# Kernel optimization log

Hardware: AMD Instinct MI355X
Metric: run time of the kernel (lower is better)

Reference implementation:

```python
import jax, jax.numpy as jnp
import numpy as np

N, E, H, ED, TD = 10000, 320000, 128, 64, 32

def _lin(x, w, b):
    return x @ w + b

def _ln(x, g, b, eps=1e-5):
    m = jnp.mean(x, axis=-1, keepdims=True)
    v = jnp.var(x, axis=-1, keepdims=True)
    return (x - m) * jax.lax.rsqrt(v + eps) * g + b

def _mlp(x, w1, b1, g, bt, w2, b2):
    y = jax.nn.silu(_ln(_lin(x, w1, b1), g, bt))
    return _lin(y, w2, b2)

def setup_inputs() -> dict:
    key = jax.random.key(0)
    ks = jax.random.split(key, 32)
    s = 0.02
    nrm = lambda k, shp: jax.random.normal(k, shp, jnp.float32) * s
    d = {}
    d['h'] = jax.random.normal(ks[0], (N, H), jnp.float32)
    d['edge_attr'] = jax.random.normal(ks[1], (E, ED), jnp.float32)
    d['edge_time_emb'] = jax.random.normal(ks[2], (E, TD), jnp.float32)
    d['edge_index'] = jax.random.randint(ks[3], (2, E), 0, N)
    # edge_emb + edge_norm
    d['w_ee'] = nrm(ks[4], (ED + TD, ED)); d['b_ee'] = jnp.zeros((ED,), jnp.float32)
    d['g_en'] = jnp.ones((ED + TD,), jnp.float32); d['bt_en'] = jnp.zeros((ED + TD,), jnp.float32)
    # node_linear / bond_linear
    d['w_nl'] = nrm(ks[5], (H, H)); d['b_nl'] = jnp.zeros((H,), jnp.float32)
    d['w_bl'] = nrm(ks[6], (ED, H)); d['b_bl'] = jnp.zeros((H,), jnp.float32)
    # bond_linear_left/right, node_linear_left/right
    d['w_bll'] = nrm(ks[7], (ED, H)); d['b_bll'] = jnp.zeros((H,), jnp.float32)
    d['w_blr'] = nrm(ks[8], (ED, H)); d['b_blr'] = jnp.zeros((H,), jnp.float32)
    d['w_nll'] = nrm(ks[9], (H, H)); d['b_nll'] = jnp.zeros((H,), jnp.float32)
    d['w_nlr'] = nrm(ks[10], (H, H)); d['b_nlr'] = jnp.zeros((H,), jnp.float32)
    # left / right MLPs: Linear(2H,H), LayerNorm(H), SiLU, Linear(H,H)
    d['mlpl_w1'] = nrm(ks[11], (2 * H, H)); d['mlpl_b1'] = jnp.zeros((H,), jnp.float32)
    d['mlpl_g'] = jnp.ones((H,), jnp.float32); d['mlpl_bt'] = jnp.zeros((H,), jnp.float32)
    d['mlpl_w2'] = nrm(ks[12], (H, H)); d['mlpl_b2'] = jnp.zeros((H,), jnp.float32)
    d['mlpr_w1'] = nrm(ks[13], (2 * H, H)); d['mlpr_b1'] = jnp.zeros((H,), jnp.float32)
    d['mlpr_g'] = jnp.ones((H,), jnp.float32); d['mlpr_bt'] = jnp.zeros((H,), jnp.float32)
    d['mlpr_w2'] = nrm(ks[14], (H, H)); d['mlpr_b2'] = jnp.zeros((H,), jnp.float32)
    # layer_norm(3H) + bond_out: Linear(3H,H), SiLU, Linear(H,ED)
    d['g_ln'] = jnp.ones((3 * H,), jnp.float32); d['bt_ln'] = jnp.zeros((3 * H,), jnp.float32)
    d['w_o1'] = nrm(ks[15], (3 * H, H)); d['b_o1'] = jnp.zeros((H,), jnp.float32)
    d['w_o2'] = nrm(ks[16], (H, ED)); d['b_o2'] = jnp.zeros((ED,), jnp.float32)
    return d

def reference(h, edge_attr, edge_time_emb, edge_index,
              w_ee, b_ee, g_en, bt_en, w_nl, b_nl, w_bl, b_bl,
              w_bll, b_bll, w_blr, b_blr, w_nll, b_nll, w_nlr, b_nlr,
              mlpl_w1, mlpl_b1, mlpl_g, mlpl_bt, mlpl_w2, mlpl_b2,
              mlpr_w1, mlpr_b1, mlpr_g, mlpr_bt, mlpr_w2, mlpr_b2,
              g_ln, bt_ln, w_o1, b_o1, w_o2, b_o2):
    src, dst = edge_index[0], edge_index[1]
    n = h.shape[0]
    # edge_attr = edge_emb(edge_norm(cat([edge_attr, edge_time_emb])))
    ea = _lin(_ln(jnp.concatenate([edge_attr, edge_time_emb], axis=-1), g_en, bt_en), w_ee, b_ee)
    # node linears applied per-node then gathered (same math as gather-then-linear)
    x_i = _lin(h, w_nll, b_nll)[src]            # [E, H]
    x_j = _lin(h, w_nlr, b_nlr)[dst]            # [E, H]
    edge_i = _lin(ea, w_bll, b_bll)             # [E, H]
    edge_j = _lin(ea, w_blr, b_blr)             # [E, H]
    inter_i = _mlp(jnp.concatenate([edge_i, x_i], axis=-1), mlpl_w1, mlpl_b1, mlpl_g, mlpl_bt, mlpl_w2, mlpl_b2)
    inter_j = _mlp(jnp.concatenate([edge_j, x_j], axis=-1), mlpr_w1, mlpr_b1, mlpr_g, mlpr_bt, mlpr_w2, mlpr_b2)
    # scatter_sum to nodes, then regather on the same index
    inter_i = jax.ops.segment_sum(inter_i, src, num_segments=n)[src]
    inter_j = jax.ops.segment_sum(inter_j, dst, num_segments=n)[dst]
    h_node = _lin(h, w_nl, b_nl)
    h_bond = jnp.concatenate([inter_i + inter_j, h_node[src] + h_node[dst], _lin(ea, w_bl, b_bl)], axis=-1)  # [E, 3H]
    h_bond = _ln(h_bond, g_ln, bt_ln)
    out = _lin(jax.nn.silu(_lin(h_bond, w_o1, b_o1)), w_o2, b_o2)  # [E, ED]
    return out
```

## Files before the change

### kernel.cpp

```cpp
#include <hip/hip_runtime.h>
#include <math.h>


using u16 = unsigned short;
using u32 = unsigned int;
typedef __attribute__((ext_vector_type(8))) short  short8;
typedef __attribute__((ext_vector_type(4))) float  f32x4;
typedef __attribute__((ext_vector_type(4))) u32    uint4v;
typedef __attribute__((ext_vector_type(2))) u32    uint2v;

constexpr int NN = 10000;
constexpr int EE = 320000;
constexpr int MAXDEG = 96;

__device__ __forceinline__ float b2f(u16 v) {
  return __builtin_bit_cast(float, (u32)v << 16);
}
__device__ __forceinline__ u16 f2b(float f) {
  u32 u = __builtin_bit_cast(u32, f);
  return (u16)((u + 0x7fffu + ((u >> 16) & 1u)) >> 16);
}
__device__ __forceinline__ uint2v pack4(f32x4 v) {
  uint2v r;
  r.x = (u32)f2b(v[0]) | ((u32)f2b(v[1]) << 16);
  r.y = (u32)f2b(v[2]) | ((u32)f2b(v[3]) << 16);
  return r;
}

struct Params {
  const void* h; const void* edge_attr; const void* te;
  const int* eidx;
  const int* flag;
  const u16 *b_ee, *g_en, *bt_en;
  const u16 *b_nl, *b_bl, *b_bll, *b_blr, *b_nll, *b_nlr;
  const u16 *l_b1, *l_g, *l_bt, *l_b2;
  const u16 *r_b1, *r_g, *r_bt, *r_b2;
  const u16 *g_ln, *bt_ln, *b_o1, *b_o2;
  const u16 *w_eeT, *w_blT, *w_bllT, *w_blrT, *w_nlT, *w_nllT, *w_nlrT;
  const u16 *l_w1T, *l_w2T, *r_w1T, *r_w2T, *o1T, *o2T;
  u16 *a_nll, *a_nlr, *h_node, *ea_ws;
  u32 *cnt0, *cnt1, *elist0, *elist1;
  u16 *accb_i, *accb_j;
  float *accf_i, *accf_j;
  u16 *inter0, *inter1;
  int amode;
  void *out;
};

__global__ __launch_bounds__(256) void k_sniff(const u16* p, int* flag)
{
  __shared__ int c;
  if (threadIdx.x == 0) c = 0;
  __syncthreads();
  u16 v = p[threadIdx.x * 2];
  int e = (v >> 7) & 0xff;
  if (e >= 100 && e <= 140) atomicAdd(&c, 1);
  __syncthreads();
  if (threadIdx.x == 0) *flag = (c >= 200) ? 1 : 0;
}

template<int K, int CT, int RT>
__device__ __forceinline__ void wave_gemm(const u16* A, int SA,
                                          const u16* __restrict__ BT,
                                          f32x4 (&acc)[RT][CT], int n0)
{
  const int lane = threadIdx.x & 63;
  const int quad = lane >> 4, l16 = lane & 15;
#pragma unroll
  for (int kt = 0; kt < K / 32; ++kt) {
    const int k0 = kt * 32 + quad * 8;
    short8 b[CT];
#pragma unroll
    for (int c = 0; c < CT; ++c)
      b[c] = *(const short8*)(BT + (size_t)(n0 + c * 16 + l16) * K + k0);
#pragma unroll
    for (int rt = 0; rt < RT; ++rt) {
      short8 av = *(const short8*)(A + (rt * 16 + l16) * SA + k0);
#pragma unroll
      for (int c = 0; c < CT; ++c)
        acc[rt][c] = __builtin_amdgcn_mfma_f32_16x16x32_bf16(av, b[c], acc[rt][c], 0, 0, 0);
    }
  }
}

template<int CT, int RT, bool SILU>
__device__ __forceinline__ void epi_lds(f32x4 (&acc)[RT][CT], u16* O, int SO,
                                        int outc0, const u16* __restrict__ bias,
                                        int biasc0)
{
  const int lane = threadIdx.x & 63;
  const int quad = lane >> 4, l16 = lane & 15;
#pragma unroll
  for (int c = 0; c < CT; ++c) {
    float bv = b2f(bias[biasc0 + c * 16 + l16]);
#pragma unroll
    for (int rt = 0; rt < RT; ++rt) {
#pragma unroll
      for (int r = 0; r < 4; ++r) {
        float v = acc[rt][c][r] + bv;
        if (SILU) v = v / (1.f + __expf(-v));
        O[(rt * 16 + quad * 4 + r) * SO + outc0 + c * 16 + l16] = f2b(v);
      }
    }
  }
}

template<int D, int ROWS, bool SILU>
__device__ __forceinline__ void ln_rows(u16* buf, int S,
                                        const u16* __restrict__ g,
                                        const u16* __restrict__ bt, float* red)
{
  constexpr int P = 256 / ROWS;
  constexpr int C = D / P;
  const int t = threadIdx.x;
  const int row = t / P, p = t % P;
  u16* r = buf + row * S + p * C;
  float s = 0.f, ss = 0.f;
#pragma unroll 8
  for (int i = 0; i < C; ++i) { float v = b2f(r[i]); s += v; ss += v * v; }
  red[row * 2 * P + p] = s;
  red[row * 2 * P + P + p] = ss;
  __syncthreads();
  float S1 = 0.f, S2 = 0.f;
#pragma unroll
  for (int q = 0; q < P; ++q) {
    S1 += red[row * 2 * P + q];
    S2 += red[row * 2 * P + P + q];
  }
  const float mean = S1 / (float)D;
  const float var  = S2 / (float)D - mean * mean;
  const float rstd = rsqrtf(var + 1e-5f);
#pragma unroll 8
  for (int i = 0; i < C; ++i) {
    int col = p * C + i;
    float v = (b2f(r[i]) - mean) * rstd * b2f(g[col]) + b2f(bt[col]);
    if (SILU) v = v / (1.f + __expf(-v));
    r[i] = f2b(v);
  }
  __syncthreads();
}

struct TDesc { const void* s; u16* d; int K; int N; };
struct TArgs { TDesc t[34]; const int* flag; };

__global__ __launch_bounds__(256) void k_transpose(TArgs a)
{
  const int flag = *a.flag;
  TDesc dsc = a.t[blockIdx.y];
  const int total = dsc.K * dsc.N;
  for (int i = blockIdx.x * 256 + threadIdx.x; i < total; i += gridDim.x * 256) {
    int n = i / dsc.K;
    int k = i - n * dsc.K;
    size_t si = (size_t)k * dsc.N + n;
    dsc.d[i] = flag ? ((const u16*)dsc.s)[si] : f2b(((const float*)dsc.s)[si]);
  }
}

__global__ __launch_bounds__(256) void k_hist(const int* eidx, u32* cnt0,
                                              u32* elist0, u32* cnt1, u32* elist1)
{
  int e = blockIdx.x * 256 + threadIdx.x;
  if (e >= EE) return;
  int n0 = eidx[e];
  u32 p0 = atomicAdd(&cnt0[n0], 1u);
  if (p0 < MAXDEG) elist0[(size_t)n0 * MAXDEG + p0] = (u32)e;
  int n1 = eidx[EE + e];
  u32 p1 = atomicAdd(&cnt1[n1], 1u);
  if (p1 < MAXDEG) elist1[(size_t)n1 * MAXDEG + p1] = (u32)e;
}

__global__ __launch_bounds__(256) void k_node(Params a)
{
  __shared__ __align__(16) u16 hs[64 * 136];
  const int tid = threadIdx.x, w = tid >> 6;
  const int n0 = blockIdx.x * 64;
  const int flag = *a.flag;
  if (flag) {
    for (int c = tid; c < 1024; c += 256) {
      int row = c >> 4, cc = c & 15;
      int node = n0 + row;
      uint4v v = {};
      if (node < NN) v = *(const uint4v*)((const u16*)a.h + (size_t)node * 128 + cc * 8);
      *(uint4v*)&hs[row * 136 + cc * 8] = v;
    }
  } else {
    for (int c = tid; c < 2048; c += 256) {
      int row = c >> 5, cc = c & 31;
      int node = n0 + row;
      uint2v pk = {};
      if (node < NN) {
        f32x4 fv = *(const f32x4*)((const float*)a.h + (size_t)node * 128 + cc * 4);
        pk = pack4(fv);
      }
      *(uint2v*)&hs[row * 136 + cc * 4] = pk;
    }
  }
  __syncthreads();
  const u16* wT[3] = { a.w_nllT, a.w_nlrT, a.w_nlT };
  const u16* bs[3] = { a.b_nll, a.b_nlr, a.b_nl };
  u16* os[3] = { a.a_nll, a.a_nlr, a.h_node };
  const int lane = tid & 63, quad = lane >> 4, l16 = lane & 15;
#pragma unroll 1
  for (int m = 0; m < 3; ++m) {
    f32x4 acc[4][2] = {};
    wave_gemm<128, 2, 4>(hs, 136, wT[m], acc, w * 32);
#pragma unroll
    for (int c = 0; c < 2; ++c) {
      int col = w * 32 + c * 16 + l16;
      float bv = b2f(bs[m][col]);
#pragma unroll
      for (int rt = 0; rt < 4; ++rt) {
#pragma unroll
        for (int r = 0; r < 4; ++r) {
          int node = n0 + rt * 16 + quad * 4 + r;
          if (node < NN) os[m][(size_t)node * 128 + col] = f2b(acc[rt][c][r] + bv);
        }
      }
    }
  }
}

__global__ __launch_bounds__(256) void k_ea(Params a)
{
  __shared__ __align__(16) u16 u[64 * 104];
  __shared__ __align__(16) u16 eas[64 * 72];
  __shared__ float red[512];
  const int tid = threadIdx.x, w = tid >> 6;
  const int e0 = blockIdx.x * 64;
  const int flag = *a.flag;
  if (flag) {
    for (int c = tid; c < 512; c += 256) {
      int row = c >> 3, cc = c & 7;
      *(uint4v*)&u[row * 104 + cc * 8] =
          *(const uint4v*)((const u16*)a.edge_attr + (size_t)(e0 + row) * 64 + cc * 8);
    }
    {
      int row = tid >> 2, cc = tid & 3;
      *(uint4v*)&u[row * 104 + 64 + cc * 8] =
          *(const uint4v*)((const u16*)a.te + (size_t)(e0 + row) * 32 + cc * 8);
    }
  } else {
    for (int c = tid; c < 1024; c += 256) {
      int row = c >> 4, cc = c & 15;
      f32x4 fv = *(const f32x4*)((const float*)a.edge_attr + (size_t)(e0 + row) * 64 + cc * 4);
      *(uint2v*)&u[row * 104 + cc * 4] = pack4(fv);
    }
    for (int c = tid; c < 512; c += 256) {
      int row = c >> 3, cc = c & 7;
      f32x4 fv = *(const f32x4*)((const float*)a.te + (size_t)(e0 + row) * 32 + cc * 4);
      *(uint2v*)&u[row * 104 + 64 + cc * 4] = pack4(fv);
    }
  }
  __syncthreads();
  ln_rows<96, 64, false>(u, 104, a.g_en, a.bt_en, red);
  {
    f32x4 acc[4][1] = {};
    wave_gemm<96, 1, 4>(u, 104, a.w_eeT, acc, w * 16);
    epi_lds<1, 4, false>(acc, eas, 72, w * 16, a.b_ee, w * 16);
  }
  __syncthreads();
  for (int c = tid; c < 512; c += 256) {
    int row = c >> 3, cc = c & 7;
    *(uint4v*)(a.ea_ws + (size_t)(e0 + row) * 64 + cc * 8) =
        *(const uint4v*)&eas[row * 72 + cc * 8];
  }
}

template<bool ATOMIC>
__global__ __launch_bounds__(256) void k_mlp(
    const u16* __restrict__ ea_ws, const int* __restrict__ eidx_side,
    const u16* __restrict__ an, const u16* __restrict__ wbT,
    const u16* __restrict__ bb, const u16* __restrict__ w1T,
    const u16* __restrict__ b1, const u16* __restrict__ gg,
    const u16* __restrict__ bt, const u16* __restrict__ w2T,
    const u16* __restrict__ b2, u16* __restrict__ inter,
    float* __restrict__ accf)
{
  __shared__ __align__(16) u16 u[64 * 264];
  __shared__ __align__(16) u16 eas[64 * 72];
  __shared__ float red[512];
  __shared__ int sidx[64];
  const int tid = threadIdx.x, w = tid >> 6;
  const int e0 = blockIdx.x * 64;
  const int lane = tid & 63, quad = lane >> 4, l16 = lane & 15;

  if (tid < 64) sidx[tid] = eidx_side[e0 + tid];
  for (int c = tid; c < 512; c += 256) {
    int row = c >> 3, cc = c & 7;
    *(uint4v*)&eas[row * 72 + cc * 8] =
        *(const uint4v*)(ea_ws + (size_t)(e0 + row) * 64 + cc * 8);
  }
  __syncthreads();
  for (int c = tid; c < 1024; c += 256) {
    int row = c >> 4, cc = c & 15;
    *(uint4v*)&u[row * 264 + 128 + cc * 8] =
        *(const uint4v*)(an + (size_t)sidx[row] * 128 + cc * 8);
  }
  {
    f32x4 acc[4][2] = {};
    wave_gemm<64, 2, 4>(eas, 72, wbT, acc, w * 32);
    epi_lds<2, 4, false>(acc, u, 264, w * 32, bb, w * 32);
  }
  __syncthreads();
  {
    f32x4 acc[4][2] = {};
    wave_gemm<256, 2, 4>(u, 264, w1T, acc, w * 32);
    __syncthreads();
    epi_lds<2, 4, false>(acc, u, 264, w * 32, b1, w * 32);
  }
  __syncthreads();
  ln_rows<128, 64, true>(u, 264, gg, bt, red);
  {
    f32x4 acc[4][2] = {};
    wave_gemm<128, 2, 4>(u, 264, w2T, acc, w * 32);
    if (ATOMIC) {
#pragma unroll
      for (int c = 0; c < 2; ++c) {
        int col = w * 32 + c * 16 + l16;
        float bias = b2f(b2[col]);
#pragma unroll
        for (int rt = 0; rt < 4; ++rt)
#pragma unroll
          for (int r = 0; r < 4; ++r) {
            int row = rt * 16 + quad * 4 + r;
            unsafeAtomicAdd(accf + (size_t)sidx[row] * 128 + col,
                            acc[rt][c][r] + bias);
          }
      }
    } else {
      epi_lds<2, 4, false>(acc, u, 264, 128 + w * 32, b2, w * 32);
      __syncthreads();
      for (int c = tid; c < 1024; c += 256) {
        int row = c >> 4, cc = c & 15;
        *(uint4v*)(inter + (size_t)(e0 + row) * 128 + cc * 8) =
            *(const uint4v*)&u[row * 264 + 128 + cc * 8];
      }
    }
  }
}

__global__ __launch_bounds__(256) void k_nodesum(const u16* __restrict__ inter,
                                                 const u32* __restrict__ cnt,
                                                 const u32* __restrict__ elist,
                                                 u16* __restrict__ accb)
{
  const int wv = (blockIdx.x * 256 + threadIdx.x) >> 6;
  const int lane = threadIdx.x & 63;
  if (wv >= NN) return;
  u32 deg = cnt[wv];
  if (deg > MAXDEG) deg = MAXDEG;
  const u32* el = elist + (size_t)wv * MAXDEG;
  float s0 = 0.f, s1 = 0.f;
  for (u32 d = 0; d < deg; ++d) {
    u32 e = el[d];
    u32 v = *(const u32*)(inter + (size_t)e * 128 + lane * 2);
    s0 += b2f((u16)(v & 0xffff));
    s1 += b2f((u16)(v >> 16));
  }
  *(u32*)(accb + (size_t)wv * 128 + lane * 2) = (u32)f2b(s0) | ((u32)f2b(s1) << 16);
}

__global__ __launch_bounds__(256) void k_stage2(Params a)
{
  __shared__ __align__(16) u16 bond[32 * 392];
  __shared__ __align__(16) u16 eas[32 * 72];
  __shared__ float red[512];
  __shared__ int sidx[2][32];
  const int tid = threadIdx.x, w = tid >> 6;
  const int e0 = blockIdx.x * 32;
  const int flag = *a.flag;
  const int lane = tid & 63, quad = lane >> 4, l16 = lane & 15;

  if (tid < 64) {
    int side = tid >> 5, i = tid & 31;
    sidx[side][i] = a.eidx[(size_t)side * EE + e0 + i];
  }
  {
    int row = tid >> 3, cc = tid & 7;
    *(uint4v*)&eas[row * 72 + cc * 8] =
        *(const uint4v*)(a.ea_ws + (size_t)(e0 + row) * 64 + cc * 8);
  }
  __syncthreads();
  if (a.amode) {
    for (int c = tid; c < 1024; c += 256) {
      int row = c >> 5, cc = c & 31;
      uint2v vi = *(const uint2v*)(a.accb_i + (size_t)sidx[0][row] * 128 + cc * 4);
      uint2v vj = *(const uint2v*)(a.accb_j + (size_t)sidx[1][row] * 128 + cc * 4);
      uint2v ov;
#pragma unroll
      for (int q = 0; q < 2; ++q) {
        float lo = b2f((u16)(vi[q] & 0xffff)) + b2f((u16)(vj[q] & 0xffff));
        float hi = b2f((u16)(vi[q] >> 16))    + b2f((u16)(vj[q] >> 16));
        ov[q] = (u32)f2b(lo) | ((u32)f2b(hi) << 16);
      }
      *(uint2v*)&bond[row * 392 + cc * 4] = ov;
    }
  } else {
    for (int c = tid; c < 1024; c += 256) {
      int row = c >> 5, cc = c & 31;
      f32x4 vi = *(const f32x4*)(a.accf_i + (size_t)sidx[0][row] * 128 + cc * 4);
      f32x4 vj = *(const f32x4*)(a.accf_j + (size_t)sidx[1][row] * 128 + cc * 4);
      f32x4 sm = vi + vj;
      *(uint2v*)&bond[row * 392 + cc * 4] = pack4(sm);
    }
  }
  for (int c = tid; c < 512; c += 256) {
    int row = c >> 4, cc = c & 15;
    uint4v hs = *(const uint4v*)(a.h_node + (size_t)sidx[0][row] * 128 + cc * 8);
    uint4v hd = *(const uint4v*)(a.h_node + (size_t)sidx[1][row] * 128 + cc * 8);
    uint4v ov;
#pragma unroll
    for (int q = 0; q < 4; ++q) {
      float lo = b2f((u16)(hs[q] & 0xffff)) + b2f((u16)(hd[q] & 0xffff));
      float hi = b2f((u16)(hs[q] >> 16))    + b2f((u16)(hd[q] >> 16));
      ov[q] = (u32)f2b(lo) | ((u32)f2b(hi) << 16);
    }
    *(uint4v*)&bond[row * 392 + 128 + cc * 8] = ov;
  }
  {
    f32x4 acc[2][2] = {};
    wave_gemm<64, 2, 2>(eas, 72, a.w_blT, acc, w * 32);
    epi_lds<2, 2, false>(acc, bond, 392, 256 + w * 32, a.b_bl, w * 32);
  }
  __syncthreads();
  ln_rows<384, 32, false>(bond, 392, a.g_ln, a.bt_ln, red);
  {
    f32x4 acc[2][2] = {};
    wave_gemm<384, 2, 2>(bond, 392, a.o1T, acc, w * 32);
    __syncthreads();
    epi_lds<2, 2, true>(acc, bond, 392, w * 32, a.b_o1, w * 32);
  }
  __syncthreads();
  {
    f32x4 acc[2][1] = {};
    wave_gemm<128, 1, 2>(bond, 392, a.o2T, acc, w * 16);
    if (flag) {
      epi_lds<1, 2, false>(acc, bond, 392, 128 + w * 16, a.b_o2, w * 16);
      __syncthreads();
      for (int c = tid; c < 256; c += 256) {
        int row = c >> 3, cc = c & 7;
        *(uint4v*)((u16*)a.out + (size_t)(e0 + row) * 64 + cc * 8) =
            *(const uint4v*)&bond[row * 392 + 128 + cc * 8];
      }
    } else {
      float bvv = b2f(a.b_o2[w * 16 + l16]);
#pragma unroll
      for (int rt = 0; rt < 2; ++rt)
#pragma unroll
        for (int r = 0; r < 4; ++r) {
          int row = rt * 16 + quad * 4 + r;
          ((float*)((char*)bond + (size_t)row * 784 + 272))[w * 16 + l16] =
              acc[rt][0][r] + bvv;
        }
      __syncthreads();
      for (int c = tid; c < 512; c += 256) {
        int row = c >> 4, cc = c & 15;
        f32x4 v = *(const f32x4*)((char*)bond + (size_t)row * 784 + 272 + cc * 16);
        *(f32x4*)((float*)a.out + (size_t)(e0 + row) * 64 + cc * 4) = v;
      }
    }
  }
}

extern "C" void kernel_launch(void* const* d_in, const int* in_sizes, int n_in,
                              void* d_out, int out_size, void* d_ws, size_t ws_size,
                              hipStream_t stream)
{
  char* ws = (char*)d_ws;

  const size_t O_EET  = 0;
  const size_t O_BLT  = 12288;
  const size_t O_BLLT = O_BLT  + 16384;
  const size_t O_BLRT = O_BLLT + 16384;
  const size_t O_NLT  = O_BLRT + 16384;
  const size_t O_NLLT = O_NLT  + 32768;
  const size_t O_NLRT = O_NLLT + 32768;
  const size_t O_LW1T = O_NLRT + 32768;
  const size_t O_LW2T = O_LW1T + 65536;
  const size_t O_RW1T = O_LW2T + 32768;
  const size_t O_RW2T = O_RW1T + 65536;
  const size_t O_O1T  = O_RW2T + 32768;
  const size_t O_O2T  = O_O1T  + 98304;
  const size_t PRM    = O_O2T  + 16384;
  const size_t FLAG   = PRM + 6016;
  const size_t A_NLL  = PRM + 6144;
  const size_t A_NLR  = A_NLL + 2560000;
  const size_t H_NODE = A_NLR + 2560000;
  const size_t EA     = H_NODE + 2560000;
  const size_t TAIL   = EA + 40960000;
  const size_t ACCF_I = TAIL;
  const size_t ACCF_J = TAIL + 5120000;
  const size_t NEED_ATOM = TAIL + 10240000;
  const size_t CNT0   = TAIL;
  const size_t CNT1   = TAIL + 40960;
  const size_t EL0    = TAIL + 81920;
  const size_t EL1    = EL0 + 3840000;
  const size_t ACCB_I = EL1 + 3840000;
  const size_t ACCB_J = ACCB_I + 2560000;
  const size_t INTER0 = ACCB_J + 2560000;
  const size_t NEED_CSR = INTER0 + 81920000;
  if (ws_size < NEED_ATOM) return;
  const int amode = (ws_size >= NEED_CSR) ? 1 : 0;

  const size_t pOff[21] = { 0, 128, 320, 512, 768, 1024, 1280, 1536, 1792,
                            2048, 2304, 2560, 2816, 3072, 3328, 3584, 3840,
                            4096, 4864, 5632, 5888 };
  const int   pIdx[21] = { 5, 6, 7, 9, 11, 13, 15, 17, 19,
                           21, 22, 23, 25, 27, 28, 29, 31,
                           32, 33, 35, 37 };
  const int   pLen[21] = { 64, 96, 96, 128, 128, 128, 128, 128, 128,
                           128, 128, 128, 128, 128, 128, 128, 128,
                           384, 384, 128, 64 };
  auto P = [&](int slot) { return (const u16*)(ws + PRM + pOff[slot]); };

  Params a;
  a.h = d_in[0]; a.edge_attr = d_in[1]; a.te = d_in[2];
  a.eidx = (const int*)d_in[3];
  a.flag = (const int*)(ws + FLAG);
  a.b_ee = P(0); a.g_en = P(1); a.bt_en = P(2);
  a.b_nl = P(3); a.b_bl = P(4); a.b_bll = P(5); a.b_blr = P(6);
  a.b_nll = P(7); a.b_nlr = P(8);
  a.l_b1 = P(9); a.l_g = P(10); a.l_bt = P(11); a.l_b2 = P(12);
  a.r_b1 = P(13); a.r_g = P(14); a.r_bt = P(15); a.r_b2 = P(16);
  a.g_ln = P(17); a.bt_ln = P(18); a.b_o1 = P(19); a.b_o2 = P(20);
  a.w_eeT = (const u16*)(ws + O_EET);   a.w_blT  = (const u16*)(ws + O_BLT);
  a.w_bllT = (const u16*)(ws + O_BLLT); a.w_blrT = (const u16*)(ws + O_BLRT);
  a.w_nlT = (const u16*)(ws + O_NLT);   a.w_nllT = (const u16*)(ws + O_NLLT);
  a.w_nlrT = (const u16*)(ws + O_NLRT);
  a.l_w1T = (const u16*)(ws + O_LW1T);  a.l_w2T = (const u16*)(ws + O_LW2T);
  a.r_w1T = (const u16*)(ws + O_RW1T);  a.r_w2T = (const u16*)(ws + O_RW2T);
  a.o1T = (const u16*)(ws + O_O1T);     a.o2T = (const u16*)(ws + O_O2T);
  a.a_nll = (u16*)(ws + A_NLL); a.a_nlr = (u16*)(ws + A_NLR);
  a.h_node = (u16*)(ws + H_NODE); a.ea_ws = (u16*)(ws + EA);
  a.cnt0 = (u32*)(ws + CNT0); a.cnt1 = (u32*)(ws + CNT1);
  a.elist0 = (u32*)(ws + EL0); a.elist1 = (u32*)(ws + EL1);
  a.accb_i = (u16*)(ws + ACCB_I); a.accb_j = (u16*)(ws + ACCB_J);
  a.accf_i = (float*)(ws + ACCF_I); a.accf_j = (float*)(ws + ACCF_J);
  a.inter0 = (u16*)(ws + INTER0); a.inter1 = (u16*)(ws + INTER0);
  a.amode = amode;
  a.out = d_out;

  TArgs ta;
  ta.flag = (const int*)(ws + FLAG);
  ta.t[0]  = { d_in[4],  (u16*)(ws + O_EET),  96, 64 };
  ta.t[1]  = { d_in[10], (u16*)(ws + O_BLT),  64, 128 };
  ta.t[2]  = { d_in[12], (u16*)(ws + O_BLLT), 64, 128 };
  ta.t[3]  = { d_in[14], (u16*)(ws + O_BLRT), 64, 128 };
  ta.t[4]  = { d_in[8],  (u16*)(ws + O_NLT),  128, 128 };
  ta.t[5]  = { d_in[16], (u16*)(ws + O_NLLT), 128, 128 };
  ta.t[6]  = { d_in[18], (u16*)(ws + O_NLRT), 128, 128 };
  ta.t[7]  = { d_in[20], (u16*)(ws + O_LW1T), 256, 128 };
  ta.t[8]  = { d_in[24], (u16*)(ws + O_LW2T), 128, 128 };
  ta.t[9]  = { d_in[26], (u16*)(ws + O_RW1T), 256, 128 };
  ta.t[10] = { d_in[30], (u16*)(ws + O_RW2T), 128, 128 };
  ta.t[11] = { d_in[34], (u16*)(ws + O_O1T),  384, 128 };
  ta.t[12] = { d_in[36], (u16*)(ws + O_O2T),  128, 64 };
  for (int s = 0; s < 21; ++s)
    ta.t[13 + s] = { d_in[pIdx[s]], (u16*)(ws + PRM + pOff[s]), 1, pLen[s] };

  k_sniff<<<1, 256, 0, stream>>>((const u16*)d_in[1], (int*)(ws + FLAG));
  if (amode) hipMemsetAsync(ws + CNT0, 0, 81920, stream);
  else       hipMemsetAsync(ws + ACCF_I, 0, 10240000, stream);
  k_transpose<<<dim3(16, 34), 256, 0, stream>>>(ta);
  if (amode)
    k_hist<<<(EE + 255) / 256, 256, 0, stream>>>(a.eidx, a.cnt0, a.elist0, a.cnt1, a.elist1);
  k_node<<<(NN + 63) / 64, 256, 0, stream>>>(a);
  k_ea<<<EE / 64, 256, 0, stream>>>(a);

  if (amode) {
    k_mlp<false><<<EE / 64, 256, 0, stream>>>(a.ea_ws, a.eidx, a.a_nll, a.w_bllT,
        a.b_bll, a.l_w1T, a.l_b1, a.l_g, a.l_bt, a.l_w2T, a.l_b2, a.inter0, nullptr);
    k_nodesum<<<(NN * 64 + 255) / 256, 256, 0, stream>>>(a.inter0, a.cnt0, a.elist0, a.accb_i);
    k_mlp<false><<<EE / 64, 256, 0, stream>>>(a.ea_ws, a.eidx + EE, a.a_nlr, a.w_blrT,
        a.b_blr, a.r_w1T, a.r_b1, a.r_g, a.r_bt, a.r_w2T, a.r_b2, a.inter1, nullptr);
    k_nodesum<<<(NN * 64 + 255) / 256, 256, 0, stream>>>(a.inter1, a.cnt1, a.elist1, a.accb_j);
  } else {
    k_mlp<true><<<EE / 64, 256, 0, stream>>>(a.ea_ws, a.eidx, a.a_nll, a.w_bllT,
        a.b_bll, a.l_w1T, a.l_b1, a.l_g, a.l_bt, a.l_w2T, a.l_b2, nullptr, a.accf_i);
    k_mlp<true><<<EE / 64, 256, 0, stream>>>(a.ea_ws, a.eidx + EE, a.a_nlr, a.w_blrT,
        a.b_blr, a.r_w1T, a.r_b1, a.r_g, a.r_bt, a.r_w2T, a.r_b2, nullptr, a.accf_j);
  }
  k_stage2<<<EE / 32, 256, 0, stream>>>(a);
}
```

Baseline: 801.5 us.

## Use hardware bf16 pack conversion, vectorize layernorm, unroll node gather-sum

Replaces the software round-to-nearest bf16 conversion with the v_cvt_pk_bf16_f32 instruction and packs pairs directly. SiLU now uses a reciprocal intrinsic instead of a divide. The layernorm helper loads and stores rows as 16-byte vectors, keeps them in registers between the two passes and reads the reduction buffer as float4. The node-sum gather is unrolled by four so more loads are in flight at once. The aim is to cut ALU instruction count and LDS traffic in the epilogues, at the cost of some register pressure and a slightly less exact reciprocal.

```diff
diff --git a/kernel.cpp b/kernel.cpp
--- a/kernel.cpp
+++ b/kernel.cpp
@@ -16,15 +16,31 @@
 __device__ __forceinline__ float b2f(u16 v) {
   return __builtin_bit_cast(float, (u32)v << 16);
 }
+__device__ __forceinline__ float b2f_lo(u32 v) {
+  return __builtin_bit_cast(float, v << 16);
+}
+__device__ __forceinline__ float b2f_hi(u32 v) {
+  return __builtin_bit_cast(float, v & 0xffff0000u);
+}
+__device__ __forceinline__ u32 cvtpk(float lo, float hi) {
+  u32 r;
+  asm("v_cvt_pk_bf16_f32 %0, %1, %2" : "=v"(r) : "v"(lo), "v"(hi));
+  return r;
+}
 __device__ __forceinline__ u16 f2b(float f) {
-  u32 u = __builtin_bit_cast(u32, f);
-  return (u16)((u + 0x7fffu + ((u >> 16) & 1u)) >> 16);
+  return (u16)cvtpk(f, f);
 }
 __device__ __forceinline__ uint2v pack4(f32x4 v) {
   uint2v r;
-  r.x = (u32)f2b(v[0]) | ((u32)f2b(v[1]) << 16);
-  r.y = (u32)f2b(v[2]) | ((u32)f2b(v[3]) << 16);
+  r.x = cvtpk(v[0], v[1]);
+  r.y = cvtpk(v[2], v[3]);
   return r;
+}
+__device__ __forceinline__ u32 addpk(u32 a, u32 b) {
+  return cvtpk(b2f_lo(a) + b2f_lo(b), b2f_hi(a) + b2f_hi(b));
+}
+__device__ __forceinline__ float silu_f(float v) {
+  return v * __builtin_amdgcn_rcpf(1.f + __expf(-v));
 }
 
 struct Params {
@@ -98,7 +114,7 @@
 #pragma unroll
       for (int r = 0; r < 4; ++r) {
         float v = acc[rt][c][r] + bv;
-        if (SILU) v = v / (1.f + __expf(-v));
+        if (SILU) v = silu_f(v);
         O[(rt * 16 + quad * 4 + r) * SO + outc0 + c * 16 + l16] = f2b(v);
       }
     }
@@ -112,30 +128,49 @@
 {
   constexpr int P = 256 / ROWS;
   constexpr int C = D / P;
+  constexpr int NV = C / 8;
   const int t = threadIdx.x;
   const int row = t / P, p = t % P;
   u16* r = buf + row * S + p * C;
+  uint4v vv[NV];
   float s = 0.f, ss = 0.f;
-#pragma unroll 8
-  for (int i = 0; i < C; ++i) { float v = b2f(r[i]); s += v; ss += v * v; }
+#pragma unroll
+  for (int n = 0; n < NV; ++n) {
+    vv[n] = *(const uint4v*)(r + n * 8);
+#pragma unroll
+    for (int q = 0; q < 4; ++q) {
+      float lo = b2f_lo(vv[n][q]), hi = b2f_hi(vv[n][q]);
+      s += lo + hi;
+      ss += lo * lo + hi * hi;
+    }
+  }
   red[row * 2 * P + p] = s;
   red[row * 2 * P + P + p] = ss;
   __syncthreads();
   float S1 = 0.f, S2 = 0.f;
 #pragma unroll
-  for (int q = 0; q < P; ++q) {
-    S1 += red[row * 2 * P + q];
-    S2 += red[row * 2 * P + P + q];
+  for (int q = 0; q < P / 4; ++q) {
+    f32x4 x = *(const f32x4*)&red[row * 2 * P + q * 4];
+    f32x4 y = *(const f32x4*)&red[row * 2 * P + P + q * 4];
+    S1 += x[0] + x[1] + x[2] + x[3];
+    S2 += y[0] + y[1] + y[2] + y[3];
   }
   const float mean = S1 / (float)D;
   const float var  = S2 / (float)D - mean * mean;
   const float rstd = rsqrtf(var + 1e-5f);
-#pragma unroll 8
-  for (int i = 0; i < C; ++i) {
-    int col = p * C + i;
-    float v = (b2f(r[i]) - mean) * rstd * b2f(g[col]) + b2f(bt[col]);
-    if (SILU) v = v / (1.f + __expf(-v));
-    r[i] = f2b(v);
+#pragma unroll
+  for (int n = 0; n < NV; ++n) {
+    uint4v gv = *(const uint4v*)(g + p * C + n * 8);
+    uint4v bv = *(const uint4v*)(bt + p * C + n * 8);
+    uint4v ov;
+#pragma unroll
+    for (int q = 0; q < 4; ++q) {
+      float lo = (b2f_lo(vv[n][q]) - mean) * rstd * b2f_lo(gv[q]) + b2f_lo(bv[q]);
+      float hi = (b2f_hi(vv[n][q]) - mean) * rstd * b2f_hi(gv[q]) + b2f_hi(bv[q]);
+      if (SILU) { lo = silu_f(lo); hi = silu_f(hi); }
+      ov[q] = cvtpk(lo, hi);
+    }
+    *(uint4v*)(r + n * 8) = ov;
   }
   __syncthreads();
 }
@@ -351,13 +386,23 @@
   if (deg > MAXDEG) deg = MAXDEG;
   const u32* el = elist + (size_t)wv * MAXDEG;
   float s0 = 0.f, s1 = 0.f;
-  for (u32 d = 0; d < deg; ++d) {
+  u32 d = 0;
+  for (; d + 4 <= deg; d += 4) {
+    uint4v ev = *(const uint4v*)(el + d);
+    u32 v0 = *(const u32*)(inter + (size_t)ev[0] * 128 + lane * 2);
+    u32 v1 = *(const u32*)(inter + (size_t)ev[1] * 128 + lane * 2);
+    u32 v2 = *(const u32*)(inter + (size_t)ev[2] * 128 + lane * 2);
+    u32 v3 = *(const u32*)(inter + (size_t)ev[3] * 128 + lane * 2);
+    s0 += b2f_lo(v0) + b2f_lo(v1) + b2f_lo(v2) + b2f_lo(v3);
+    s1 += b2f_hi(v0) + b2f_hi(v1) + b2f_hi(v2) + b2f_hi(v3);
+  }
+  for (; d < deg; ++d) {
     u32 e = el[d];
     u32 v = *(const u32*)(inter + (size_t)e * 128 + lane * 2);
-    s0 += b2f((u16)(v & 0xffff));
-    s1 += b2f((u16)(v >> 16));
-  }
-  *(u32*)(accb + (size_t)wv * 128 + lane * 2) = (u32)f2b(s0) | ((u32)f2b(s1) << 16);
+    s0 += b2f_lo(v);
+    s1 += b2f_hi(v);
+  }
+  *(u32*)(accb + (size_t)wv * 128 + lane * 2) = cvtpk(s0, s1);
 }
 
 __global__ __launch_bounds__(256) void k_stage2(Params a)
@@ -387,12 +432,8 @@
       uint2v vi = *(const uint2v*)(a.accb_i + (size_t)sidx[0][row] * 128 + cc * 4);
       uint2v vj = *(const uint2v*)(a.accb_j + (size_t)sidx[1][row] * 128 + cc * 4);
       uint2v ov;
-#pragma unroll
-      for (int q = 0; q < 2; ++q) {
-        float lo = b2f((u16)(vi[q] & 0xffff)) + b2f((u16)(vj[q] & 0xffff));
-        float hi = b2f((u16)(vi[q] >> 16))    + b2f((u16)(vj[q] >> 16));
-        ov[q] = (u32)f2b(lo) | ((u32)f2b(hi) << 16);
-      }
+      ov.x = addpk(vi.x, vj.x);
+      ov.y = addpk(vi.y, vj.y);
       *(uint2v*)&bond[row * 392 + cc * 4] = ov;
     }
   } else {
@@ -410,11 +451,7 @@
     uint4v hd = *(const uint4v*)(a.h_node + (size_t)sidx[1][row] * 128 + cc * 8);
     uint4v ov;
 #pragma unroll
-    for (int q = 0; q < 4; ++q) {
-      float lo = b2f((u16)(hs[q] & 0xffff)) + b2f((u16)(hd[q] & 0xffff));
-      float hi = b2f((u16)(hs[q] >> 16))    + b2f((u16)(hd[q] >> 16));
-      ov[q] = (u32)f2b(lo) | ((u32)f2b(hi) << 16);
-    }
+    for (int q = 0; q < 4; ++q) ov[q] = addpk(hs[q], hd[q]);
     *(uint4v*)&bond[row * 392 + 128 + cc * 8] = ov;
   }
   {
```

After: 745.2 us. -7.0%, faster.
